# Kernel optimization log

Hardware: AMD Instinct MI355X
Metric: run time of the kernel (lower is better)

## Reference

```python
import jax, jax.numpy as jnp
import numpy as np

N_NODES = 100000
N_EDGES = 1600000
IN_F = 128
OUT_F = 32
HEADS = 4
NEG_SLOPE = 0.2
EPS = 1e-8


def setup_inputs() -> dict:
    key = jax.random.key(0)
    k1, k2, k3, k4 = jax.random.split(key, 4)
    x = jax.random.normal(k1, (N_NODES, IN_F), dtype=jnp.float32)
    # torch Linear weight layout: [out_features*num_heads, in_features]
    # xavier_uniform-like scale
    limW = float(np.sqrt(6.0 / (IN_F + OUT_F * HEADS)))
    W = jax.random.uniform(k2, (OUT_F * HEADS, IN_F), dtype=jnp.float32, minval=-limW, maxval=limW)
    lima = float(np.sqrt(6.0 / (HEADS + 2 * OUT_F)))
    a = jax.random.uniform(k3, (HEADS, 2 * OUT_F), dtype=jnp.float32, minval=-lima, maxval=lima)
    edge_index = jax.random.randint(k4, (2, N_EDGES), 0, N_NODES, dtype=jnp.int64)
    return {"x": x, "W": W, "a": a, "edge_index": edge_index}


def reference(x, W, a, edge_index):
    # x: [N, in], W: [H*F, in], a: [H, 2F], edge_index: [2, E]
    N = x.shape[0]
    H = HEADS
    F = OUT_F
    h = (x @ W.T).reshape(N, H, F)                      # [N, H, F]
    src, dst = edge_index[0], edge_index[1]
    h_src = h[src]                                       # [E, H, F]
    h_dst = h[dst]                                       # [E, H, F]
    # (cat([h_src, h_dst], -1) * a).sum(-1) == h_src@a_src + h_dst@a_dst
    a_src, a_dst = a[:, :F], a[:, F:]
    att = jnp.einsum('ehf,hf->eh', h_src, a_src) + jnp.einsum('ehf,hf->eh', h_dst, a_dst)  # [E, H]
    att = jnp.where(att >= 0, att, NEG_SLOPE * att)      # leaky_relu(0.2)
    att = jnp.exp(att - att.max())                       # global-max stabilization (as in source)
    att_sum = jax.ops.segment_sum(att, dst, num_segments=N)    # [N, H]
    att = att / (att_sum[dst] + EPS)                     # segment softmax
    # dropout is identity in eval mode
    out = jax.ops.segment_sum(att[..., None] * h_src, dst, num_segments=N)  # [N, H, F]
    return out.reshape(N, H * F)                         # concat=True
```

## Files before the change

kernel.cpp:

```cpp
#include <hip/hip_runtime.h>
#include <hip/hip_bf16.h>

#define NEG_SLOPE 0.2f
#define EPSV 1e-8f
#define BCAP 5632

typedef float f32x4 __attribute__((ext_vector_type(4)));
typedef short bf16x8 __attribute__((ext_vector_type(8)));
typedef unsigned short us8 __attribute__((ext_vector_type(8)));

static __device__ __forceinline__ float bf16tof(unsigned short s) {
    union { unsigned u; float f; } c; c.u = ((unsigned)s) << 16; return c.f;
}
static __device__ __forceinline__ unsigned short ftobf16(float f) {
    __hip_bfloat16 b = __float2bfloat16(f);
    return *(unsigned short*)&b;
}
static __device__ __forceinline__ float leaky_exp(float v) {
    v = fmaxf(v, NEG_SLOPE * v);
    return __expf(v);
}

__global__ __launch_bounds__(256, 2) void k_gemm(
        const float* __restrict__ x, const float* __restrict__ W,
        const float* __restrict__ a, unsigned short* __restrict__ h_bf,
        float* __restrict__ asrc, float* __restrict__ adst, int N) {
    __shared__ unsigned short xs[128 * 128];
    __shared__ unsigned short ws[128 * 128];
    __shared__ float sa[256];
    int tid = threadIdx.x;
    int nb = blockIdx.x * 128;

    sa[tid] = a[tid];

#pragma unroll
    for (int it = 0; it < 16; ++it) {
        int f = tid + 256 * it;
        int row = f >> 5;
        int k0 = (f & 31) << 2;
        int sw = row * 128 + (k0 ^ ((row & 7) << 3));
        int n = nb + row; if (n >= N) n = N - 1;
        float4 v = *(const float4*)(x + (size_t)n * 128 + k0);
        ushort4 o;
        o.x = ftobf16(v.x); o.y = ftobf16(v.y);
        o.z = ftobf16(v.z); o.w = ftobf16(v.w);
        *(ushort4*)&xs[sw] = o;
        float4 wv = *(const float4*)(W + (size_t)row * 128 + k0);
        ushort4 ow;
        ow.x = ftobf16(wv.x); ow.y = ftobf16(wv.y);
        ow.z = ftobf16(wv.z); ow.w = ftobf16(wv.w);
        *(ushort4*)&ws[sw] = ow;
    }
    __syncthreads();

    int w  = tid >> 6;
    int l  = tid & 63;
    int lr = l & 15;
    int lg = l >> 4;

    f32x4 acc[2][8];
    {
        f32x4 zz = {0.f, 0.f, 0.f, 0.f};
#pragma unroll
        for (int nt = 0; nt < 2; ++nt)
#pragma unroll
            for (int jt = 0; jt < 8; ++jt)
                acc[nt][jt] = zz;
    }

#pragma unroll
    for (int ks = 0; ks < 4; ++ks) {
        int kofs = ks * 32 + lg * 8;
        bf16x8 xf[2];
#pragma unroll
        for (int nt = 0; nt < 2; ++nt) {
            int row = w * 32 + nt * 16 + lr;
            xf[nt] = *(const bf16x8*)&xs[row * 128 + (kofs ^ ((row & 7) << 3))];
        }
#pragma unroll
        for (int jt = 0; jt < 8; ++jt) {
            int j = jt * 16 + lr;
            bf16x8 wf = *(const bf16x8*)&ws[j * 128 + (kofs ^ ((j & 7) << 3))];
#pragma unroll
            for (int nt = 0; nt < 2; ++nt)
                acc[nt][jt] = __builtin_amdgcn_mfma_f32_16x16x32_bf16(
                    wf, xf[nt], acc[nt][jt], 0, 0, 0);
        }
    }

#pragma unroll
    for (int g = 0; g < 4; ++g) {
        f32x4 as0 = *(const f32x4*)&sa[g * 64 +      lg * 4];
        f32x4 as1 = *(const f32x4*)&sa[g * 64 + 16 + lg * 4];
        f32x4 ad0 = *(const f32x4*)&sa[g * 64 + 32 + lg * 4];
        f32x4 ad1 = *(const f32x4*)&sa[g * 64 + 48 + lg * 4];
#pragma unroll
        for (int nt = 0; nt < 2; ++nt) {
            float ps = 0.f, pd = 0.f;
#pragma unroll
            for (int r = 0; r < 4; ++r) {
                ps += acc[nt][2 * g][r] * as0[r] + acc[nt][2 * g + 1][r] * as1[r];
                pd += acc[nt][2 * g][r] * ad0[r] + acc[nt][2 * g + 1][r] * ad1[r];
            }
            ps += __shfl_xor(ps, 16); pd += __shfl_xor(pd, 16);
            ps += __shfl_xor(ps, 32); pd += __shfl_xor(pd, 32);
            if (lg == 0) {
                int n = nb + w * 32 + nt * 16 + lr;
                if (n < N) {
                    asrc[(size_t)n * 4 + g] = ps;
                    adst[(size_t)n * 4 + g] = pd;
                }
            }
        }
    }

    __syncthreads();
#pragma unroll
    for (int nt = 0; nt < 2; ++nt) {
        int row = w * 32 + nt * 16 + lr;
        int m = (row & 7) << 3;
#pragma unroll
        for (int jt = 0; jt < 8; ++jt) {
            int j0 = jt * 16 + lg * 4;
            ushort4 o;
            o.x = ftobf16(acc[nt][jt][0]);
            o.y = ftobf16(acc[nt][jt][1]);
            o.z = ftobf16(acc[nt][jt][2]);
            o.w = ftobf16(acc[nt][jt][3]);
            *(ushort4*)&xs[row * 128 + (j0 ^ m)] = o;
        }
    }
    __syncthreads();
#pragma unroll
    for (int it = 0; it < 8; ++it) {
        int f = tid + 256 * it;
        int row = f >> 4;
        int c8 = (f & 15) << 3;
        int n = nb + row;
        if (n < N) {
            us8 v = *(const us8*)&xs[row * 128 + (c8 ^ ((row & 7) << 3))];
            *(us8*)(h_bf + (size_t)n * 128 + c8) = v;
        }
    }
}

__global__ __launch_bounds__(512) void k_bscatter(const int* __restrict__ ei,
        int* __restrict__ relcur, unsigned* __restrict__ ebuf, int E, int epb) {
    __shared__ int hist[512];
    __shared__ int wcur[512];
    __shared__ int bslot[512];
    int t = threadIdx.x;
    int lo = blockIdx.x * epb;
    int hi = min(E, lo + epb);
    hist[t] = 0;
    wcur[t] = 0;
    __syncthreads();
    int sreg[4], dreg[4];
    int cnt = 0;
#pragma unroll
    for (int k = 0; k < 4; k++) {
        int e = lo + t + 512 * k;
        if (e < hi) {
            sreg[k] = ei[e];
            dreg[k] = ei[E + e];
            atomicAdd(&hist[dreg[k] >> 8], 1);
            cnt = k + 1;
        }
    }
    __syncthreads();
    int c = hist[t];
    int res = c ? atomicAdd(&relcur[t], c) : 0;
    bslot[t] = t * BCAP + res;
    __syncthreads();
    for (int k = 0; k < cnt; k++) {
        int s = sreg[k];
        int d = dreg[k];
        int b = d >> 8;
        int off = atomicAdd(&wcur[b], 1);
        int slot = bslot[b] + off;
        if (slot < (b + 1) * BCAP)
            ebuf[slot] = ((unsigned)(d & 255) << 23) | (unsigned)s;
    }
}

__global__ __launch_bounds__(512) void k_build(const int* __restrict__ relcur,
        const unsigned* __restrict__ ebuf,
        int* __restrict__ row_ptr, int* __restrict__ csr_src,
        int NBK, int N, int E) {
    __shared__ int smA[512];
    __shared__ int hist[256];
    __shared__ int smB[256];
    __shared__ int excl[256];
    int b = blockIdx.x;
    int t = threadIdx.x;

    smA[t] = (t < NBK) ? min(relcur[t], BCAP) : 0;
    __syncthreads();
    for (int off = 1; off < 512; off <<= 1) {
        int u = (t >= off) ? smA[t - off] : 0;
        __syncthreads();
        smA[t] += u;
        __syncthreads();
    }
    int cnt  = min(relcur[b], BCAP);
    int base = smA[b] - cnt;
    if (b == 0 && t == 0) row_ptr[N] = E;

    int d0 = b << 8;
    const unsigned* ep = ebuf + (size_t)b * BCAP;

    if (t < 256) hist[t] = 0;
    __syncthreads();
    for (int i = t; i < cnt; i += 512)
        atomicAdd(&hist[ep[i] >> 23], 1);
    __syncthreads();

    int s = (t < 256) ? hist[t] : 0;
    if (t < 256) smB[t] = s;
    __syncthreads();
    for (int off = 1; off < 256; off <<= 1) {
        int u = (t >= off && t < 256) ? smB[t - off] : 0;
        __syncthreads();
        if (t < 256) smB[t] += u;
        __syncthreads();
    }
    if (t < 256) {
        int ex = smB[t] - s;
        excl[t] = ex;
        int node = d0 + t;
        if (node < N) row_ptr[node] = base + ex;
    }
    __syncthreads();

    for (int i = t; i < cnt; i += 512) {
        unsigned p = ep[i];
        int pos = base + atomicAdd(&excl[p >> 23], 1);
        csr_src[pos] = (int)(p & 0x7FFFFFu);
    }
}

__global__ __launch_bounds__(256) void k_agg(
        const int* __restrict__ row_ptr, const int* __restrict__ csr_src,
        const float* __restrict__ asrc, const float* __restrict__ adst,
        const unsigned short* __restrict__ h_bf,
        float* __restrict__ out, int N) {
    __shared__ int   se[4][2][68];
    __shared__ float sw[4][2][272];
    int tid = threadIdx.x;
    int w  = tid >> 6;
    int l  = tid & 63;
    int gg = l >> 4;
    int m  = l & 15;
    int hh = m >> 2;

    int n = blockIdx.x * 16 + w * 4 + gg;
    bool valid = (n < N);
    int nc = valid ? n : (N - 1);
    int lo  = row_ptr[nc];
    int deg = row_ptr[nc + 1] - lo;
    float4 dv = *(const float4*)(adst + 4 * (size_t)nc);

    int md = deg;
    md = max(md, __shfl_xor(md, 16));
    md = max(md, __shfl_xor(md, 32));
    int nch = (md + 15) >> 4;

    float acc[8] = {};
    float asum = 0.f;
    const unsigned short* hp = h_bf + 8 * m;

#define ACC8(U, WT) do { \
        union { unsigned u; float f; } q; \
        q.u = (U).x << 16;         acc[0] += (WT) * q.f; \
        q.u = (U).x & 0xFFFF0000u; acc[1] += (WT) * q.f; \
        q.u = (U).y << 16;         acc[2] += (WT) * q.f; \
        q.u = (U).y & 0xFFFF0000u; acc[3] += (WT) * q.f; \
        q.u = (U).z << 16;         acc[4] += (WT) * q.f; \
        q.u = (U).z & 0xFFFF0000u; acc[5] += (WT) * q.f; \
        q.u = (U).w << 16;         acc[6] += (WT) * q.f; \
        q.u = (U).w & 0xFFFF0000u; acc[7] += (WT) * q.f; \
    } while (0)

    if (m < deg) {
        int s = csr_src[lo + m];
        se[w][0][17 * gg + m] = s;
        float4 sv = *(const float4*)(asrc + 4 * (size_t)s);
        float4 wv;
        wv.x = leaky_exp(sv.x + dv.x);
        wv.y = leaky_exp(sv.y + dv.y);
        wv.z = leaky_exp(sv.z + dv.z);
        wv.w = leaky_exp(sv.w + dv.w);
        *(float4*)&sw[w][0][68 * gg + 4 * m] = wv;
    }

    for (int c = 0; c < nch; ++c) {
        int cb = c & 1;
        int sN = 0; float4 svN; bool haveN = false;
        {
            int eN = (c + 1) * 16 + m;
            if (c + 1 < nch && eN < deg) {
                sN = csr_src[lo + eN];
                svN = *(const float4*)(asrc + 4 * (size_t)sN);
                haveN = true;
            }
        }
        __builtin_amdgcn_wave_barrier();
        int base16 = c * 16;
        int cnt = min(deg - base16, 16);
        const int*   sep = &se[w][cb][17 * gg];
        const float* swp = &sw[w][cb][68 * gg];
        int i = 0;
        uint4 u0, u1;
        if (cnt >= 2) {
            u0 = *(const uint4*)(hp + (size_t)sep[0] * 128);
            u1 = *(const uint4*)(hp + (size_t)sep[1] * 128);
        }
        for (; i + 4 <= cnt; i += 2) {
            uint4 t0 = *(const uint4*)(hp + (size_t)sep[i + 2] * 128);
            uint4 t1 = *(const uint4*)(hp + (size_t)sep[i + 3] * 128);
            float w0 = swp[4 * i + hh];
            float w1 = swp[4 * i + 4 + hh];
            ACC8(u0, w0);
            ACC8(u1, w1);
            asum += w0 + w1;
            u0 = t0; u1 = t1;
        }
        if (i + 2 <= cnt) {
            float w0 = swp[4 * i + hh];
            float w1 = swp[4 * i + 4 + hh];
            ACC8(u0, w0);
            ACC8(u1, w1);
            asum += w0 + w1;
            i += 2;
        }
        for (; i < cnt; ++i) {
            int s0 = sep[i];
            float w0 = swp[4 * i + hh];
            uint4 uu = *(const uint4*)(hp + (size_t)s0 * 128);
            ACC8(uu, w0);
            asum += w0;
        }
        if (haveN) {
            se[w][cb ^ 1][17 * gg + m] = sN;
            float4 wv;
            wv.x = leaky_exp(svN.x + dv.x);
            wv.y = leaky_exp(svN.y + dv.y);
            wv.z = leaky_exp(svN.z + dv.z);
            wv.w = leaky_exp(svN.w + dv.w);
            *(float4*)&sw[w][cb ^ 1][68 * gg + 4 * m] = wv;
        }
        __builtin_amdgcn_wave_barrier();
    }
#undef ACC8

    if (valid) {
        float inv = 1.f / (asum + EPSV);
        float4 o0, o1;
        o0.x = acc[0] * inv; o0.y = acc[1] * inv;
        o0.z = acc[2] * inv; o0.w = acc[3] * inv;
        o1.x = acc[4] * inv; o1.y = acc[5] * inv;
        o1.z = acc[6] * inv; o1.w = acc[7] * inv;
        *(float4*)(out + (size_t)n * 128 + 8 * m) = o0;
        *(float4*)(out + (size_t)n * 128 + 8 * m + 4) = o1;
    }
}

extern "C" void kernel_launch(void* const* d_in, const int* in_sizes, int n_in,
                              void* d_out, int out_size, void* d_ws, size_t ws_size,
                              hipStream_t stream) {
    const float* x = (const float*)d_in[0];
    const float* W = (const float*)d_in[1];
    const float* a = (const float*)d_in[2];
    const int* ei = (const int*)d_in[3];
    float* out = (float*)d_out;

    int N = in_sizes[0] / 128;
    int E = in_sizes[3] / 2;
    int NBK = (N + 255) >> 8;

    char* wsb = (char*)d_ws;
    size_t off = 0;
    auto alloc = [&](size_t bytes) -> void* {
        void* p = wsb + off;
        off += (bytes + 255) / 256 * 256;
        return p;
    };
    unsigned short* h_bf = (unsigned short*)alloc((size_t)N * 128 * 2);
    float* asrc = (float*)alloc((size_t)N * 4 * 4);
    float* adst = (float*)alloc((size_t)N * 4 * 4);
    int* row_ptr = (int*)alloc((size_t)(N + 1) * 4);
    int* relcur = (int*)alloc(512 * 4);
    unsigned* ebuf = (unsigned*)alloc((size_t)NBK * BCAP * 4);
    int* csr_src = (int*)alloc((size_t)E * 4);

    hipMemsetAsync(relcur, 0, 512 * 4, stream);

    dim3 ggrid((N + 127) / 128);
    k_gemm<<<ggrid, 256, 0, stream>>>(x, W, a, h_bf, asrc, adst, N);
    int nsb = (E + 2047) / 2048;
    k_bscatter<<<nsb, 512, 0, stream>>>(ei, relcur, ebuf, E, 2048);
    k_build<<<NBK, 512, 0, stream>>>(relcur, ebuf, row_ptr, csr_src, NBK, N, E);
    k_agg<<<(N + 15) / 16, 256, 0, stream>>>(row_ptr, csr_src, asrc, adst, h_bf, out, N);
}
```

Baseline: 225.1 us.

## Merge GEMM and edge bucket scatter into one launch and cache ranks in build

Fuses the dense projection GEMM and the edge bucket-scatter into a single launch. Blocks are interleaved so the compute-bound GEMM and the memory/atomic-bound scatter overlap on the GPU, and one kernel launch is saved. In k_build, each thread now keeps its payloads and atomic ranks in registers from the histogram pass. This avoids re-reading ebuf and a second round of shared atomics when writing the CSR. In exchange, scatter blocks inherit the GEMM's large shared-memory footprint and 256-thread shape, which limits their occupancy, and k_build uses more registers.

```diff
diff --git a/kernel.cpp b/kernel.cpp
--- a/kernel.cpp
+++ b/kernel.cpp
@@ -21,16 +21,66 @@
     return __expf(v);
 }
 
-__global__ __launch_bounds__(256, 2) void k_gemm(
+__global__ __launch_bounds__(256, 2) void k_gemm_scatter(
         const float* __restrict__ x, const float* __restrict__ W,
         const float* __restrict__ a, unsigned short* __restrict__ h_bf,
-        float* __restrict__ asrc, float* __restrict__ adst, int N) {
+        float* __restrict__ asrc, float* __restrict__ adst,
+        const int* __restrict__ ei, int* __restrict__ relcur,
+        unsigned* __restrict__ ebuf, int E, int N, int GB, int SB) {
     __shared__ unsigned short xs[128 * 128];
     __shared__ unsigned short ws[128 * 128];
     __shared__ float sa[256];
     int tid = threadIdx.x;
-    int nb = blockIdx.x * 128;
-
+    int bid = blockIdx.x;
+
+    int M = min(GB, SB);
+    bool isGemm; int myIdx;
+    if (bid < 2 * M) { isGemm = ((bid & 1) == 0); myIdx = bid >> 1; }
+    else { isGemm = (GB > SB); myIdx = bid - M; }
+
+    if (!isGemm) {
+        int* hist  = (int*)xs;
+        int* wcur  = hist + 512;
+        int* bslot = wcur + 512;
+        int lo = myIdx * 2048;
+        int hi = min(E, lo + 2048);
+        hist[tid] = 0; hist[tid + 256] = 0;
+        wcur[tid] = 0; wcur[tid + 256] = 0;
+        __syncthreads();
+        int sreg[8], dreg[8];
+#pragma unroll
+        for (int k = 0; k < 8; k++) {
+            int e = lo + tid + 256 * k;
+            if (e < hi) {
+                sreg[k] = ei[e];
+                dreg[k] = ei[E + e];
+                atomicAdd(&hist[dreg[k] >> 8], 1);
+            }
+        }
+        __syncthreads();
+        int c0 = hist[tid], c1 = hist[tid + 256];
+        int r0 = c0 ? atomicAdd(&relcur[tid], c0) : 0;
+        int r1 = c1 ? atomicAdd(&relcur[tid + 256], c1) : 0;
+        bslot[tid]       = tid * BCAP + r0;
+        bslot[tid + 256] = (tid + 256) * BCAP + r1;
+        __syncthreads();
+#pragma unroll
+        for (int k = 0; k < 8; k++) {
+            int e = lo + tid + 256 * k;
+            if (e < hi) {
+                int s = sreg[k];
+                int d = dreg[k];
+                int b = d >> 8;
+                int off = atomicAdd(&wcur[b], 1);
+                int slot = bslot[b] + off;
+                if (slot < (b + 1) * BCAP)
+                    ebuf[slot] = ((unsigned)(d & 255) << 23) | (unsigned)s;
+            }
+        }
+        return;
+    }
+
+    int nb = myIdx * 128;
     sa[tid] = a[tid];
 
 #pragma unroll
@@ -144,45 +194,6 @@
     }
 }
 
-__global__ __launch_bounds__(512) void k_bscatter(const int* __restrict__ ei,
-        int* __restrict__ relcur, unsigned* __restrict__ ebuf, int E, int epb) {
-    __shared__ int hist[512];
-    __shared__ int wcur[512];
-    __shared__ int bslot[512];
-    int t = threadIdx.x;
-    int lo = blockIdx.x * epb;
-    int hi = min(E, lo + epb);
-    hist[t] = 0;
-    wcur[t] = 0;
-    __syncthreads();
-    int sreg[4], dreg[4];
-    int cnt = 0;
-#pragma unroll
-    for (int k = 0; k < 4; k++) {
-        int e = lo + t + 512 * k;
-        if (e < hi) {
-            sreg[k] = ei[e];
-            dreg[k] = ei[E + e];
-            atomicAdd(&hist[dreg[k] >> 8], 1);
-            cnt = k + 1;
-        }
-    }
-    __syncthreads();
-    int c = hist[t];
-    int res = c ? atomicAdd(&relcur[t], c) : 0;
-    bslot[t] = t * BCAP + res;
-    __syncthreads();
-    for (int k = 0; k < cnt; k++) {
-        int s = sreg[k];
-        int d = dreg[k];
-        int b = d >> 8;
-        int off = atomicAdd(&wcur[b], 1);
-        int slot = bslot[b] + off;
-        if (slot < (b + 1) * BCAP)
-            ebuf[slot] = ((unsigned)(d & 255) << 23) | (unsigned)s;
-    }
-}
-
 __global__ __launch_bounds__(512) void k_build(const int* __restrict__ relcur,
         const unsigned* __restrict__ ebuf,
         int* __restrict__ row_ptr, int* __restrict__ csr_src,
@@ -190,7 +201,6 @@
     __shared__ int smA[512];
     __shared__ int hist[256];
     __shared__ int smB[256];
-    __shared__ int excl[256];
     int b = blockIdx.x;
     int t = threadIdx.x;
 
@@ -211,8 +221,19 @@
 
     if (t < 256) hist[t] = 0;
     __syncthreads();
-    for (int i = t; i < cnt; i += 512)
-        atomicAdd(&hist[ep[i] >> 23], 1);
+    unsigned pay[11]; int rnk[11];
+#pragma unroll
+    for (int k = 0; k < 11; ++k) {
+        int i = t + 512 * k;
+        if (i < cnt) {
+            unsigned p = ep[i];
+            pay[k] = p;
+            rnk[k] = atomicAdd(&hist[p >> 23], 1);
+        } else {
+            pay[k] = 0u;
+            rnk[k] = -1;
+        }
+    }
     __syncthreads();
 
     int s = (t < 256) ? hist[t] : 0;
@@ -226,16 +247,18 @@
     }
     if (t < 256) {
         int ex = smB[t] - s;
-        excl[t] = ex;
+        hist[t] = ex;
         int node = d0 + t;
         if (node < N) row_ptr[node] = base + ex;
     }
     __syncthreads();
 
-    for (int i = t; i < cnt; i += 512) {
-        unsigned p = ep[i];
-        int pos = base + atomicAdd(&excl[p >> 23], 1);
-        csr_src[pos] = (int)(p & 0x7FFFFFu);
+#pragma unroll
+    for (int k = 0; k < 11; ++k) {
+        if (rnk[k] >= 0) {
+            unsigned p = pay[k];
+            csr_src[base + hist[p >> 23] + rnk[k]] = (int)(p & 0x7FFFFFu);
+        }
     }
 }
 
@@ -395,10 +418,10 @@
 
     hipMemsetAsync(relcur, 0, 512 * 4, stream);
 
-    dim3 ggrid((N + 127) / 128);
-    k_gemm<<<ggrid, 256, 0, stream>>>(x, W, a, h_bf, asrc, adst, N);
-    int nsb = (E + 2047) / 2048;
-    k_bscatter<<<nsb, 512, 0, stream>>>(ei, relcur, ebuf, E, 2048);
+    int GB = (N + 127) / 128;
+    int SB = (E + 2047) / 2048;
+    k_gemm_scatter<<<GB + SB, 256, 0, stream>>>(x, W, a, h_bf, asrc, adst,
+                                                ei, relcur, ebuf, E, N, GB, SB);
     k_build<<<NBK, 512, 0, stream>>>(relcur, ebuf, row_ptr, csr_src, NBK, N, E);
     k_agg<<<(N + 15) / 16, 256, 0, stream>>>(row_ptr, csr_src, asrc, adst, h_bf, out, N);
 }
```

Result: faster. 212.1 us (-5.8%).

## Fuse CSR build and aggregation into one cooperative persistent kernel

Applied to the files above, without the earlier changes.

Replaces the bucket-scatter, CSR-build and aggregation kernels with a single cooperative kernel. It does a global degree histogram with atomics, a two-level prefix scan, an atomic scatter into CSR, then a grid-strided aggregation, with grid.sync between phases. This removes launches, the memset and the intermediate bucket buffer. In exchange it uses global atomics on random destinations, which are likely more contended than the shared-memory bucketed version, adds several grid-wide barriers, and assumes 256 CUs when sizing the grid.

```diff
diff --git a/kernel.cpp b/kernel.cpp
--- a/kernel.cpp
+++ b/kernel.cpp
@@ -1,17 +1,16 @@
 #include <hip/hip_runtime.h>
 #include <hip/hip_bf16.h>
+#include <hip/hip_cooperative_groups.h>
 
 #define NEG_SLOPE 0.2f
 #define EPSV 1e-8f
-#define BCAP 5632
+
+namespace cg = cooperative_groups;
 
 typedef float f32x4 __attribute__((ext_vector_type(4)));
 typedef short bf16x8 __attribute__((ext_vector_type(8)));
 typedef unsigned short us8 __attribute__((ext_vector_type(8)));
 
-static __device__ __forceinline__ float bf16tof(unsigned short s) {
-    union { unsigned u; float f; } c; c.u = ((unsigned)s) << 16; return c.f;
-}
 static __device__ __forceinline__ unsigned short ftobf16(float f) {
     __hip_bfloat16 b = __float2bfloat16(f);
     return *(unsigned short*)&b;
@@ -144,129 +143,93 @@
     }
 }
 
-__global__ __launch_bounds__(512) void k_bscatter(const int* __restrict__ ei,
-        int* __restrict__ relcur, unsigned* __restrict__ ebuf, int E, int epb) {
-    __shared__ int hist[512];
-    __shared__ int wcur[512];
-    __shared__ int bslot[512];
-    int t = threadIdx.x;
-    int lo = blockIdx.x * epb;
-    int hi = min(E, lo + epb);
-    hist[t] = 0;
-    wcur[t] = 0;
-    __syncthreads();
-    int sreg[4], dreg[4];
-    int cnt = 0;
-#pragma unroll
-    for (int k = 0; k < 4; k++) {
-        int e = lo + t + 512 * k;
-        if (e < hi) {
-            sreg[k] = ei[e];
-            dreg[k] = ei[E + e];
-            atomicAdd(&hist[dreg[k] >> 8], 1);
-            cnt = k + 1;
-        }
-    }
-    __syncthreads();
-    int c = hist[t];
-    int res = c ? atomicAdd(&relcur[t], c) : 0;
-    bslot[t] = t * BCAP + res;
-    __syncthreads();
-    for (int k = 0; k < cnt; k++) {
-        int s = sreg[k];
-        int d = dreg[k];
-        int b = d >> 8;
-        int off = atomicAdd(&wcur[b], 1);
-        int slot = bslot[b] + off;
-        if (slot < (b + 1) * BCAP)
-            ebuf[slot] = ((unsigned)(d & 255) << 23) | (unsigned)s;
-    }
-}
-
-__global__ __launch_bounds__(512) void k_build(const int* __restrict__ relcur,
-        const unsigned* __restrict__ ebuf,
-        int* __restrict__ row_ptr, int* __restrict__ csr_src,
-        int NBK, int N, int E) {
-    __shared__ int smA[512];
-    __shared__ int hist[256];
-    __shared__ int smB[256];
-    __shared__ int excl[256];
+__global__ __launch_bounds__(256) void k_coop(
+        const int* __restrict__ ei,
+        const float* __restrict__ asrc, const float* __restrict__ adst,
+        const unsigned short* __restrict__ h_bf, float* __restrict__ out,
+        int* __restrict__ row_ptr, int* __restrict__ cur,
+        int* __restrict__ bsum, int* __restrict__ csr_src,
+        int E, int N) {
+    cg::grid_group grid = cg::this_grid();
+    __shared__ int sm[256];
+    __shared__ int   se[4][2][68];
+    __shared__ float swb[4][2][272];
     int b = blockIdx.x;
     int t = threadIdx.x;
-
-    smA[t] = (t < NBK) ? min(relcur[t], BCAP) : 0;
-    __syncthreads();
-    for (int off = 1; off < 512; off <<= 1) {
-        int u = (t >= off) ? smA[t - off] : 0;
+    int G = gridDim.x;
+    int T = G * 256;
+    int gtid = b * 256 + t;
+
+    for (int i = gtid; i < N; i += T) cur[i] = 0;
+    grid.sync();
+
+    for (int e = gtid; e < E; e += T)
+        atomicAdd(&cur[ei[E + e]], 1);
+    grid.sync();
+
+    int SEG = (N + G - 1) / G;
+    int base = b * SEG;
+    int carry = 0;
+    for (int off = 0; off < SEG; off += 256) {
+        int i = base + off + t;
+        bool ok = (off + t < SEG) && (i < N);
+        int v = ok ? cur[i] : 0;
+        sm[t] = v; __syncthreads();
+        for (int s = 1; s < 256; s <<= 1) {
+            int u = (t >= s) ? sm[t - s] : 0; __syncthreads();
+            sm[t] += u; __syncthreads();
+        }
+        if (ok) row_ptr[i] = carry + sm[t] - v;
+        carry += sm[255];
         __syncthreads();
-        smA[t] += u;
-        __syncthreads();
-    }
-    int cnt  = min(relcur[b], BCAP);
-    int base = smA[b] - cnt;
-    if (b == 0 && t == 0) row_ptr[N] = E;
-
-    int d0 = b << 8;
-    const unsigned* ep = ebuf + (size_t)b * BCAP;
-
-    if (t < 256) hist[t] = 0;
-    __syncthreads();
-    for (int i = t; i < cnt; i += 512)
-        atomicAdd(&hist[ep[i] >> 23], 1);
-    __syncthreads();
-
-    int s = (t < 256) ? hist[t] : 0;
-    if (t < 256) smB[t] = s;
-    __syncthreads();
-    for (int off = 1; off < 256; off <<= 1) {
-        int u = (t >= off && t < 256) ? smB[t - off] : 0;
-        __syncthreads();
-        if (t < 256) smB[t] += u;
-        __syncthreads();
-    }
-    if (t < 256) {
-        int ex = smB[t] - s;
-        excl[t] = ex;
-        int node = d0 + t;
-        if (node < N) row_ptr[node] = base + ex;
-    }
-    __syncthreads();
-
-    for (int i = t; i < cnt; i += 512) {
-        unsigned p = ep[i];
-        int pos = base + atomicAdd(&excl[p >> 23], 1);
-        csr_src[pos] = (int)(p & 0x7FFFFFu);
-    }
-}
-
-__global__ __launch_bounds__(256) void k_agg(
-        const int* __restrict__ row_ptr, const int* __restrict__ csr_src,
-        const float* __restrict__ asrc, const float* __restrict__ adst,
-        const unsigned short* __restrict__ h_bf,
-        float* __restrict__ out, int N) {
-    __shared__ int   se[4][2][68];
-    __shared__ float sw[4][2][272];
-    int tid = threadIdx.x;
-    int w  = tid >> 6;
-    int l  = tid & 63;
-    int gg = l >> 4;
+    }
+    if (t == 0) bsum[b] = carry;
+    grid.sync();
+
+    if (b == 0) {
+        int c2 = 0;
+        for (int off = 0; off < G; off += 256) {
+            int i = off + t;
+            int v = (i < G) ? bsum[i] : 0;
+            sm[t] = v; __syncthreads();
+            for (int s = 1; s < 256; s <<= 1) {
+                int u = (t >= s) ? sm[t - s] : 0; __syncthreads();
+                sm[t] += u; __syncthreads();
+            }
+            if (i < G) bsum[i] = c2 + sm[t] - v;
+            c2 += sm[255];
+            __syncthreads();
+        }
+    }
+    grid.sync();
+
+    {
+        int boff = bsum[b];
+        for (int off = 0; off < SEG; off += 256) {
+            int i = base + off + t;
+            if ((off + t < SEG) && (i < N)) {
+                int rp = row_ptr[i] + boff;
+                row_ptr[i] = rp;
+                cur[i] = rp;
+            }
+        }
+        if (b == 0 && t == 0) row_ptr[N] = E;
+    }
+    grid.sync();
+
+    for (int e = gtid; e < E; e += T) {
+        int s = ei[e];
+        int d = ei[E + e];
+        int pos = atomicAdd(&cur[d], 1);
+        csr_src[pos] = s;
+    }
+    grid.sync();
+
+    int w  = t >> 6;
+    int l  = t & 63;
+    int sg = l >> 4;
     int m  = l & 15;
     int hh = m >> 2;
-
-    int n = blockIdx.x * 16 + w * 4 + gg;
-    bool valid = (n < N);
-    int nc = valid ? n : (N - 1);
-    int lo  = row_ptr[nc];
-    int deg = row_ptr[nc + 1] - lo;
-    float4 dv = *(const float4*)(adst + 4 * (size_t)nc);
-
-    int md = deg;
-    md = max(md, __shfl_xor(md, 16));
-    md = max(md, __shfl_xor(md, 32));
-    int nch = (md + 15) >> 4;
-
-    float acc[8] = {};
-    float asum = 0.f;
     const unsigned short* hp = h_bf + 8 * m;
 
 #define ACC8(U, WT) do { \
@@ -281,88 +244,107 @@
         q.u = (U).w & 0xFFFF0000u; acc[7] += (WT) * q.f; \
     } while (0)
 
-    if (m < deg) {
-        int s = csr_src[lo + m];
-        se[w][0][17 * gg + m] = s;
-        float4 sv = *(const float4*)(asrc + 4 * (size_t)s);
-        float4 wv;
-        wv.x = leaky_exp(sv.x + dv.x);
-        wv.y = leaky_exp(sv.y + dv.y);
-        wv.z = leaky_exp(sv.z + dv.z);
-        wv.w = leaky_exp(sv.w + dv.w);
-        *(float4*)&sw[w][0][68 * gg + 4 * m] = wv;
-    }
-
-    for (int c = 0; c < nch; ++c) {
-        int cb = c & 1;
-        int sN = 0; float4 svN; bool haveN = false;
-        {
-            int eN = (c + 1) * 16 + m;
-            if (c + 1 < nch && eN < deg) {
-                sN = csr_src[lo + eN];
-                svN = *(const float4*)(asrc + 4 * (size_t)sN);
-                haveN = true;
-            }
+    int NG = (N + 15) >> 4;
+    for (int grp = b; grp < NG; grp += G) {
+        int n = grp * 16 + w * 4 + sg;
+        bool valid = (n < N);
+        int nc = valid ? n : (N - 1);
+        int lo  = row_ptr[nc];
+        int deg = row_ptr[nc + 1] - lo;
+        float4 dv = *(const float4*)(adst + 4 * (size_t)nc);
+
+        int md = deg;
+        md = max(md, __shfl_xor(md, 16));
+        md = max(md, __shfl_xor(md, 32));
+        int nch = (md + 15) >> 4;
+
+        float acc[8] = {};
+        float asum = 0.f;
+
+        if (m < deg) {
+            int s = csr_src[lo + m];
+            se[w][0][17 * sg + m] = s;
+            float4 sv = *(const float4*)(asrc + 4 * (size_t)s);
+            float4 wv;
+            wv.x = leaky_exp(sv.x + dv.x);
+            wv.y = leaky_exp(sv.y + dv.y);
+            wv.z = leaky_exp(sv.z + dv.z);
+            wv.w = leaky_exp(sv.w + dv.w);
+            *(float4*)&swb[w][0][68 * sg + 4 * m] = wv;
         }
         __builtin_amdgcn_wave_barrier();
-        int base16 = c * 16;
-        int cnt = min(deg - base16, 16);
-        const int*   sep = &se[w][cb][17 * gg];
-        const float* swp = &sw[w][cb][68 * gg];
-        int i = 0;
-        uint4 u0, u1;
-        if (cnt >= 2) {
-            u0 = *(const uint4*)(hp + (size_t)sep[0] * 128);
-            u1 = *(const uint4*)(hp + (size_t)sep[1] * 128);
-        }
-        for (; i + 4 <= cnt; i += 2) {
-            uint4 t0 = *(const uint4*)(hp + (size_t)sep[i + 2] * 128);
-            uint4 t1 = *(const uint4*)(hp + (size_t)sep[i + 3] * 128);
-            float w0 = swp[4 * i + hh];
-            float w1 = swp[4 * i + 4 + hh];
-            ACC8(u0, w0);
-            ACC8(u1, w1);
-            asum += w0 + w1;
-            u0 = t0; u1 = t1;
-        }
-        if (i + 2 <= cnt) {
-            float w0 = swp[4 * i + hh];
-            float w1 = swp[4 * i + 4 + hh];
-            ACC8(u0, w0);
-            ACC8(u1, w1);
-            asum += w0 + w1;
-            i += 2;
-        }
-        for (; i < cnt; ++i) {
-            int s0 = sep[i];
-            float w0 = swp[4 * i + hh];
-            uint4 uu = *(const uint4*)(hp + (size_t)s0 * 128);
-            ACC8(uu, w0);
-            asum += w0;
-        }
-        if (haveN) {
-            se[w][cb ^ 1][17 * gg + m] = sN;
-            float4 wv;
-            wv.x = leaky_exp(svN.x + dv.x);
-            wv.y = leaky_exp(svN.y + dv.y);
-            wv.z = leaky_exp(svN.z + dv.z);
-            wv.w = leaky_exp(svN.w + dv.w);
-            *(float4*)&sw[w][cb ^ 1][68 * gg + 4 * m] = wv;
-        }
-        __builtin_amdgcn_wave_barrier();
+
+        for (int c = 0; c < nch; ++c) {
+            int cb = c & 1;
+            int sN = 0; float4 svN; bool haveN = false;
+            {
+                int eN = (c + 1) * 16 + m;
+                if (c + 1 < nch && eN < deg) {
+                    sN = csr_src[lo + eN];
+                    svN = *(const float4*)(asrc + 4 * (size_t)sN);
+                    haveN = true;
+                }
+            }
+            __builtin_amdgcn_wave_barrier();
+            int base16 = c * 16;
+            int cnt = min(deg - base16, 16);
+            const int*   sep = &se[w][cb][17 * sg];
+            const float* swp = &swb[w][cb][68 * sg];
+            int i = 0;
+            uint4 u0, u1;
+            if (cnt >= 2) {
+                u0 = *(const uint4*)(hp + (size_t)sep[0] * 128);
+                u1 = *(const uint4*)(hp + (size_t)sep[1] * 128);
+            }
+            for (; i + 4 <= cnt; i += 2) {
+                uint4 t0 = *(const uint4*)(hp + (size_t)sep[i + 2] * 128);
+                uint4 t1 = *(const uint4*)(hp + (size_t)sep[i + 3] * 128);
+                float w0 = swp[4 * i + hh];
+                float w1 = swp[4 * i + 4 + hh];
+                ACC8(u0, w0);
+                ACC8(u1, w1);
+                asum += w0 + w1;
+                u0 = t0; u1 = t1;
+            }
+            if (i + 2 <= cnt) {
+                float w0 = swp[4 * i + hh];
+                float w1 = swp[4 * i + 4 + hh];
+                ACC8(u0, w0);
+                ACC8(u1, w1);
+                asum += w0 + w1;
+                i += 2;
+            }
+            for (; i < cnt; ++i) {
+                int s0 = sep[i];
+                float w0 = swp[4 * i + hh];
+                uint4 uu = *(const uint4*)(hp + (size_t)s0 * 128);
+                ACC8(uu, w0);
+                asum += w0;
+            }
+            if (haveN) {
+                se[w][cb ^ 1][17 * sg + m] = sN;
+                float4 wv;
+                wv.x = leaky_exp(svN.x + dv.x);
+                wv.y = leaky_exp(svN.y + dv.y);
+                wv.z = leaky_exp(svN.z + dv.z);
+                wv.w = leaky_exp(svN.w + dv.w);
+                *(float4*)&swb[w][cb ^ 1][68 * sg + 4 * m] = wv;
+            }
+            __builtin_amdgcn_wave_barrier();
+        }
+
+        if (valid) {
+            float inv = 1.f / (asum + EPSV);
+            float4 o0, o1;
+            o0.x = acc[0] * inv; o0.y = acc[1] * inv;
+            o0.z = acc[2] * inv; o0.w = acc[3] * inv;
+            o1.x = acc[4] * inv; o1.y = acc[5] * inv;
+            o1.z = acc[6] * inv; o1.w = acc[7] * inv;
+            *(float4*)(out + (size_t)n * 128 + 8 * m) = o0;
+            *(float4*)(out + (size_t)n * 128 + 8 * m + 4) = o1;
+        }
     }
 #undef ACC8
-
-    if (valid) {
-        float inv = 1.f / (asum + EPSV);
-        float4 o0, o1;
-        o0.x = acc[0] * inv; o0.y = acc[1] * inv;
-        o0.z = acc[2] * inv; o0.w = acc[3] * inv;
-        o1.x = acc[4] * inv; o1.y = acc[5] * inv;
-        o1.z = acc[6] * inv; o1.w = acc[7] * inv;
-        *(float4*)(out + (size_t)n * 128 + 8 * m) = o0;
-        *(float4*)(out + (size_t)n * 128 + 8 * m + 4) = o1;
-    }
 }
 
 extern "C" void kernel_launch(void* const* d_in, const int* in_sizes, int n_in,
@@ -376,7 +358,6 @@
 
     int N = in_sizes[0] / 128;
     int E = in_sizes[3] / 2;
-    int NBK = (N + 255) >> 8;
 
     char* wsb = (char*)d_ws;
     size_t off = 0;
@@ -389,16 +370,23 @@
     float* asrc = (float*)alloc((size_t)N * 4 * 4);
     float* adst = (float*)alloc((size_t)N * 4 * 4);
     int* row_ptr = (int*)alloc((size_t)(N + 1) * 4);
-    int* relcur = (int*)alloc(512 * 4);
-    unsigned* ebuf = (unsigned*)alloc((size_t)NBK * BCAP * 4);
+    int* cur = (int*)alloc((size_t)N * 4);
+    int* bsum = (int*)alloc(4096 * 4);
     int* csr_src = (int*)alloc((size_t)E * 4);
-
-    hipMemsetAsync(relcur, 0, 512 * 4, stream);
 
     dim3 ggrid((N + 127) / 128);
     k_gemm<<<ggrid, 256, 0, stream>>>(x, W, a, h_bf, asrc, adst, N);
-    int nsb = (E + 2047) / 2048;
-    k_bscatter<<<nsb, 512, 0, stream>>>(ei, relcur, ebuf, E, 2048);
-    k_build<<<NBK, 512, 0, stream>>>(relcur, ebuf, row_ptr, csr_src, NBK, N, E);
-    k_agg<<<(N + 15) / 16, 256, 0, stream>>>(row_ptr, csr_src, asrc, adst, h_bf, out, N);
-}
+
+    int maxB = 0;
+    if (hipOccupancyMaxActiveBlocksPerMultiprocessor(&maxB, (const void*)k_coop,
+                                                     256, 0) != hipSuccess || maxB < 1)
+        maxB = 1;
+    int G = maxB * 256;
+    if (G > 4096) G = 4096;
+
+    void* kargs[] = { (void*)&ei, (void*)&asrc, (void*)&adst, (void*)&h_bf,
+                      (void*)&out, (void*)&row_ptr, (void*)&cur, (void*)&bsum,
+                      (void*)&csr_src, (void*)&E, (void*)&N };
+    hipLaunchCooperativeKernel((const void*)k_coop, dim3(G), dim3(256),
+                               kargs, 0, stream);
+}
```

Result: slower. 871.8 us (+287.2%).
